# Kernel optimization log

Measured on AMD Instinct MI355X. Metric: run time of the kernel, lower is better.

Reference implementation:

```python
import jax, jax.numpy as jnp
import numpy as np

PC_MIN = jnp.array([0.0, -39.68, -3.0], jnp.float32)
VOX = jnp.array([0.16, 0.16, 4.0], jnp.float32)
NX, NY = 432, 496  # grid cells in x and y (z grid size is 1)
MAXP = 32          # max points per pillar


def setup_inputs():
    key = jax.random.key(0)
    ks = jax.random.split(key, 16)
    B, N = 2, 16000
    u = jax.random.uniform(ks[0], (B, N, 4), dtype=jnp.float32)
    # points uniformly spread over the point-cloud range, intensity in [0,1)
    points = jnp.stack([u[..., 0] * 69.12, u[..., 1] * 79.36 - 39.68,
                        u[..., 2] * 4.0 - 3.0, u[..., 3]], axis=-1)

    def cw(k, co, ci):
        return jax.random.normal(k, (co, ci, 3, 3), jnp.float32) / np.float32(np.sqrt(ci * 9.0))

    def cws(k, L, c):
        return jax.random.normal(k, (L, c, c, 3, 3), jnp.float32) / np.float32(np.sqrt(c * 9.0))

    def st(k, shape):
        k1, k2 = jax.random.split(k)
        return (1.0 + 0.1 * jax.random.normal(k1, shape, jnp.float32),
                0.1 * jax.random.normal(k2, shape, jnp.float32))

    vfe_w = 0.1 * jax.random.normal(ks[1], (64, 10), jnp.float32)
    vfe_s, vfe_t = st(ks[2], (64,))
    b1_w0 = cw(ks[3], 4, 64);   b1_s0, b1_t0 = st(ks[4], (4,))
    b1_w = cws(ks[5], 3, 4);    b1_s, b1_t = st(ks[6], (3, 4))
    b2_w0 = cw(ks[7], 16, 4);   b2_s0, b2_t0 = st(ks[8], (16,))
    b2_w = cws(ks[9], 5, 16);   b2_s, b2_t = st(ks[10], (5, 16))
    b3_w0 = cw(ks[11], 64, 16); b3_s0, b3_t0 = st(ks[12], (64,))
    b3_w = cws(ks[13], 5, 64);  b3_s, b3_t = st(ks[14], (5, 64))
    return dict(points=points, vfe_w=vfe_w, vfe_s=vfe_s, vfe_t=vfe_t,
                b1_w0=b1_w0, b1_s0=b1_s0, b1_t0=b1_t0, b1_w=b1_w, b1_s=b1_s, b1_t=b1_t,
                b2_w0=b2_w0, b2_s0=b2_s0, b2_t0=b2_t0, b2_w=b2_w, b2_s=b2_s, b2_t=b2_t,
                b3_w0=b3_w0, b3_s0=b3_s0, b3_t0=b3_t0, b3_w=b3_w, b3_s=b3_s, b3_t=b3_t)


def _voxelize_vfe_scatter(points, vfe_w, vfe_s, vfe_t):
    """Hard voxelization (hash-bucket by pillar coord, pad to MAXP) + PillarVFE + scatter to BEV canvas."""
    B, N, C = points.shape
    V = B * N  # worst case: every point its own pillar
    pts = points.reshape(V, C)
    cid = jnp.floor((pts[:, :3] - PC_MIN) / VOX).astype(jnp.int32)
    cid = jnp.clip(cid, 0, jnp.array([NX - 1, NY - 1, 0], jnp.int32))
    bidx = jnp.repeat(jnp.arange(B, dtype=jnp.int32), N)
    # linear pillar id: b*NY*NX + y*NX + x  (z grid dim is 1 -> z idx always 0)
    gid = bidx * (NY * NX) + cid[:, 1] * NX + cid[:, 0]
    order = jnp.argsort(gid)  # stable -> preserves per-pillar point order
    g = gid[order]; p = pts[order]; c = cid[order]
    pos = jnp.arange(V, dtype=jnp.int32)
    flag = jnp.concatenate([jnp.ones((1,), bool), g[1:] != g[:-1]])
    vidx = jnp.cumsum(flag) - 1                                 # dense pillar index
    rank = pos - jax.lax.cummax(jnp.where(flag, pos, 0), axis=0)  # slot within pillar
    keep = rank < MAXP
    voxels = jnp.zeros((V, MAXP, C), points.dtype).at[vidx, rank].set(p, mode='drop')
    num = jnp.zeros((V,), jnp.int32).at[vidx].add(keep.astype(jnp.int32))
    OOB = B * NY * NX
    pillar_gid = jnp.full((V,), OOB, jnp.int32).at[vidx].set(g)  # unused slots stay out-of-bounds
    pillar_c = jnp.zeros((V, 3), jnp.int32).at[vidx].set(c)
    # PillarVFE features: [x,y,z,r, cluster offset(3), center offset(3)] = 10
    denom = jnp.maximum(num, 1).astype(points.dtype)[:, None]
    mean = jnp.zeros((V, 3), points.dtype).at[vidx].add(p[:, :3] * keep[:, None]) / denom
    f_cluster = voxels[:, :, :3] - mean[:, None, :]
    center = pillar_c.astype(points.dtype) * VOX + (VOX * 0.5 + PC_MIN)
    f_center = voxels[:, :, :3] - center[:, None, :]
    mask = (jnp.arange(MAXP)[None, :] < num[:, None])[:, :, None].astype(points.dtype)
    feat = jnp.concatenate([voxels, f_cluster, f_center], axis=-1) * mask  # (V, 32, 10)
    x = jnp.einsum('vpc,oc->vpo', feat, vfe_w)        # PFN linear (no bias)
    x = jax.nn.relu(x * vfe_s + vfe_t)                # eval-mode BN folded to scale/shift
    pillar = x.max(axis=1)                            # (V, 64) max over points
    canvas = jnp.zeros((B * NY * NX, 64), points.dtype).at[pillar_gid].set(pillar, mode='drop')
    return canvas.reshape(B, NY, NX, 64).transpose(0, 3, 1, 2)  # (B, 64, NY, NX)


def _conv_bn_relu(x, w, s, t):
    y = jax.lax.conv_general_dilated(x, w, (1, 1), [(1, 1), (1, 1)],
                                     dimension_numbers=('NCHW', 'OIHW', 'NCHW'))
    return jax.nn.relu(y * s[None, :, None, None] + t[None, :, None, None])


def _block(x, w0, s0, t0, ws, ss, ts):
    x = _conv_bn_relu(x, w0, s0, t0)
    for i in range(ws.shape[0]):  # fixed small layer count
        x = _conv_bn_relu(x, ws[i], ss[i], ts[i])
    return x


def reference(points, vfe_w, vfe_s, vfe_t,
              b1_w0, b1_s0, b1_t0, b1_w, b1_s, b1_t,
              b2_w0, b2_s0, b2_t0, b2_w, b2_s, b2_t,
              b3_w0, b3_s0, b3_t0, b3_w, b3_s, b3_t):
    bev = _voxelize_vfe_scatter(points, vfe_w, vfe_s, vfe_t)
    x1 = _block(bev, b1_w0, b1_s0, b1_t0, b1_w, b1_s, b1_t)
    x2 = _block(x1, b2_w0, b2_s0, b2_t0, b2_w, b2_s, b2_t)
    x3 = _block(x2, b3_w0, b3_s0, b3_t0, b3_w, b3_s, b3_t)
    # no deblocks (cfg lacks UPSAMPLE_STRIDES) -> concat raw block outputs: 4+16+64 = 84 ch
    return jnp.concatenate([x1, x2, x3], axis=1)  # (B, 84, 496, 432)
```

## Files before the change

kernel.cpp:

```cpp
#include <hip/hip_runtime.h>
#include <math.h>

static constexpr int H = 496, W = 432, Bn = 2, Np = 16000;
static constexpr int HW = H * W;

typedef __bf16 bf16x8 __attribute__((ext_vector_type(8)));
typedef float f32x16 __attribute__((ext_vector_type(16)));

__device__ inline void bin_xy(float px, float py, int& ix, int& iy) {
  ix = (int)floorf(px * 6.25f);
  iy = (int)floorf((py + 39.68f) * 6.25f);
  ix = min(max(ix, 0), W - 1);
  iy = min(max(iy, 0), H - 1);
}

__global__ __launch_bounds__(256)
void count_kernel(const float* __restrict__ pts, int* __restrict__ cnt,
                  float* __restrict__ sums) {
  int p = blockIdx.x * blockDim.x + threadIdx.x;
  if (p >= Bn * Np) return;
  float px = pts[p * 4 + 0], py = pts[p * 4 + 1], pz = pts[p * 4 + 2];
  int b = p / Np;
  int ix, iy;
  bin_xy(px, py, ix, iy);
  int gid = b * HW + iy * W + ix;
  atomicAdd(&cnt[gid], 1);
  atomicAdd(&sums[3 * gid + 0], px);
  atomicAdd(&sums[3 * gid + 1], py);
  atomicAdd(&sums[3 * gid + 2], pz);
}

__global__ __launch_bounds__(256)
void vfe_kernel(const float* __restrict__ pts, const int* __restrict__ cnt,
                const float* __restrict__ sums, const float* __restrict__ vw,
                const float* __restrict__ vs, const float* __restrict__ vt,
                float* __restrict__ out) {
  int tid = blockIdx.x * blockDim.x + threadIdx.x;
  if (tid >= Bn * Np * 64) return;
  int o = tid & 63;
  int p = tid >> 6;
  int b = p / Np;
  float px = pts[p * 4 + 0], py = pts[p * 4 + 1];
  float pz = pts[p * 4 + 2], pr = pts[p * 4 + 3];
  int ix, iy;
  bin_xy(px, py, ix, iy);
  int gid = b * HW + iy * W + ix;
  int n = cnt[gid];
  float denom = (float)max(n, 1);
  float mx = sums[3 * gid + 0] / denom;
  float my = sums[3 * gid + 1] / denom;
  float mz = sums[3 * gid + 2] / denom;
  float cx = (float)ix * 0.16f + 0.08f;
  float cy = (float)iy * 0.16f + (0.08f - 39.68f);
  float f[10] = {px, py, pz, pr, px - mx, py - my, pz - mz,
                 px - cx, py - cy, pz + 1.0f};
  const float* wr = vw + o * 10;
  float d = 0.f;
#pragma unroll
  for (int c = 0; c < 10; c++) d += f[c] * wr[c];
  float val = d * vs[o] + vt[o];
  val = fmaxf(val, 0.f);
  if (n < 32) val = fmaxf(val, fmaxf(vt[o], 0.f));
  unsigned int* dst = (unsigned int*)(out + (size_t)b * (84 * HW) +
                                      (size_t)(20 + o) * HW + (size_t)iy * W + ix);
  atomicMax(dst, __float_as_uint(val));
}

template <int CI, int COT>
__global__ __launch_bounds__(256)
void conv3x3(const float* __restrict__ in, int in_bs, const float* __restrict__ w,
             const float* __restrict__ s, const float* __restrict__ t,
             float* __restrict__ out, int out_bs, int npix) {
  int pix = blockIdx.x * blockDim.x + threadIdx.x;
  if (pix >= npix) return;
  int b = pix / HW;
  int rem = pix - b * HW;
  int y = rem / W;
  int x = rem - y * W;
  int co0 = blockIdx.y * COT;
  const float* inb = in + (size_t)b * in_bs;

  int offs[9];
  bool okm[9];
#pragma unroll
  for (int ky = 0; ky < 3; ky++) {
    int yy = y + ky - 1;
    bool yok = (unsigned)yy < (unsigned)H;
#pragma unroll
    for (int kx = 0; kx < 3; kx++) {
      int xx = x + kx - 1;
      okm[ky * 3 + kx] = yok && ((unsigned)xx < (unsigned)W);
      offs[ky * 3 + kx] = yy * W + xx;
    }
  }
  float acc[COT];
#pragma unroll
  for (int i = 0; i < COT; i++) acc[i] = 0.f;
  for (int ci = 0; ci < CI; ci++) {
    const float* ip = inb + (size_t)ci * HW;
    float iv[9];
#pragma unroll
    for (int k = 0; k < 9; k++) iv[k] = okm[k] ? ip[offs[k]] : 0.f;
    const float* wp = w + ((size_t)co0 * CI + ci) * 9;
#pragma unroll
    for (int cg = 0; cg < COT; cg++) {
      const float* wc = wp + (size_t)cg * CI * 9;
#pragma unroll
      for (int k = 0; k < 9; k++) acc[cg] = fmaf(iv[k], wc[k], acc[cg]);
    }
  }
  float* ob = out + (size_t)b * out_bs + (size_t)rem;
#pragma unroll
  for (int cg = 0; cg < COT; cg++) {
    float v = acc[cg] * s[co0 + cg] + t[co0 + cg];
    ob[(size_t)(co0 + cg) * HW] = fmaxf(v, 0.f);
  }
}

__global__ __launch_bounds__(256)
void prepack(const float* __restrict__ w0, const float* __restrict__ ws,
             __bf16* __restrict__ wt) {
  int idx = blockIdx.x * 256 + threadIdx.x;
  const int E0 = 64 * 144, EN = 64 * 576;
  if (idx < E0) {
    int blk = idx >> 9, rem = idx & 511;
    int tp = blk >> 1, nt = blk & 1;
    int co = nt * 32 + (rem >> 4);
    int ci = rem & 15;
    int ky = tp / 3, kx = tp - ky * 3;
    wt[idx] = (__bf16)w0[((co * 16 + ci) * 3 + ky) * 3 + kx];
  } else {
    int j = idx - E0;
    if (j >= 5 * EN) return;
    int n = j / EN, rr = j - n * EN;
    int blk = rr >> 9, rem = rr & 511;
    int tpkc = blk >> 1, nt = blk & 1;
    int tp = tpkc >> 2, kc = tpkc & 3;
    int co = nt * 32 + (rem >> 4);
    int ci = kc * 16 + (rem & 15);
    int ky = tp / 3, kx = tp - ky * 3;
    wt[idx] = (__bf16)ws[n * 36864 + ((co * 64 + ci) * 3 + ky) * 3 + kx];
  }
}

__global__ __launch_bounds__(256)
void cvt_nhwc16(const float* __restrict__ x2, __bf16* __restrict__ n16) {
  int q = blockIdx.x * 256 + threadIdx.x;
  if (q >= Bn * HW) return;
  int b = q / HW;
  int p = q - b * HW;
  const float* x2b = x2 + (size_t)b * 84 * HW;
  __bf16* nb = n16 + (size_t)b * 84 * HW * 2;
  __bf16 v[16];
#pragma unroll
  for (int ci = 0; ci < 16; ci++) v[ci] = (__bf16)x2b[(size_t)ci * HW + p];
  *(bf16x8*)(nb + (size_t)p * 16) = *(bf16x8*)v;
  *(bf16x8*)(nb + (size_t)p * 16 + 8) = *(bf16x8*)(v + 8);
}

template <int CI, bool FINAL>
__global__ __launch_bounds__(256, 3)
void mconv(const __bf16* __restrict__ in, size_t in_bstride,
           const __bf16* __restrict__ wt, const float* __restrict__ s,
           const float* __restrict__ t, __bf16* __restrict__ outb,
           size_t outb_bstride, float* __restrict__ outf, size_t outf_bstride) {
  constexpr int KC = CI / 16;
  constexpr int PADW = (CI == 64) ? 72 : 24;
  constexpr int HALO_B = 324 * PADW * 2;
  constexpr int TRAN_B = FINAL ? 128 * 66 * 4 : 0;
  constexpr int SMEM_B = HALO_B > TRAN_B ? HALO_B : TRAN_B;
  __shared__ __align__(16) char smem[SMEM_B];
  __bf16* hl = (__bf16*)smem;

  const int tid = threadIdx.x;
  const int bz = blockIdx.y;
  const int ty = blockIdx.x / 27, tx = blockIdx.x - ty * 27;
  const int y0 = ty * 16, x0 = tx * 16;
  in += (size_t)bz * in_bstride;

  constexpr int NCH = CI / 8;
  constexpr int TOT = 324 * NCH;
  for (int q = tid; q < TOT; q += 256) {
    int hp = q / NCH, c8 = q - hp * NCH;
    int hy = hp / 18, hx = hp - hy * 18;
    int gy = y0 - 1 + hy, gx = x0 - 1 + hx;
    int4 v = {0, 0, 0, 0};
    if ((unsigned)gy < (unsigned)H && (unsigned)gx < (unsigned)W)
      v = *(const int4*)(in + (size_t)(gy * W + gx) * CI + c8 * 8);
    *(int4*)(hl + hp * PADW + c8 * 8) = v;
  }
  __syncthreads();

  const int lane = tid & 63;
  const int wv = tid >> 6;
  const int col = lane & 31, half = lane >> 5;
  const int ly0 = 4 * wv + (col >> 4);
  const int lx = col & 15;

  f32x16 z = {0.f, 0.f, 0.f, 0.f, 0.f, 0.f, 0.f, 0.f,
              0.f, 0.f, 0.f, 0.f, 0.f, 0.f, 0.f, 0.f};
  f32x16 a00 = z, a01 = z, a10 = z, a11 = z;

  const int laneoff = col * 16 + half * 8;
  const __bf16* wbase = wt + laneoff;

#pragma unroll
  for (int tp = 0; tp < 9; ++tp) {
    const __bf16* a0r = hl + ((ly0 + tp / 3) * 18 + lx + tp % 3) * PADW + half * 8;
    const __bf16* a1r = a0r + 2 * 18 * PADW;
    const __bf16* bb = wbase + ((tp * KC) << 10);
#pragma unroll
    for (int kc = 0; kc < KC; ++kc) {
      bf16x8 af0 = *(const bf16x8*)(a0r + kc * 16);
      bf16x8 af1 = *(const bf16x8*)(a1r + kc * 16);
      bf16x8 b0 = *(const bf16x8*)(bb + (kc << 10));
      bf16x8 b1 = *(const bf16x8*)(bb + (kc << 10) + 512);
      a00 = __builtin_amdgcn_mfma_f32_32x32x16_bf16(af0, b0, a00, 0, 0, 0);
      a01 = __builtin_amdgcn_mfma_f32_32x32x16_bf16(af0, b1, a01, 0, 0, 0);
      a10 = __builtin_amdgcn_mfma_f32_32x32x16_bf16(af1, b0, a10, 0, 0, 0);
      a11 = __builtin_amdgcn_mfma_f32_32x32x16_bf16(af1, b1, a11, 0, 0, 0);
    }
  }

  float s0 = s[col], t0v = t[col], s1 = s[col + 32], t1v = t[col + 32];
  if constexpr (!FINAL) {
    __bf16* ob = outb + (size_t)bz * outb_bstride;
#pragma unroll
    for (int r = 0; r < 16; ++r) {
      int row = (r & 3) + 8 * (r >> 2) + 4 * half;
      int py = y0 + 4 * wv + (row >> 4);
      int px = x0 + (row & 15);
      size_t gp0 = (size_t)py * W + px;
      size_t gp1 = gp0 + (size_t)2 * W;
      ob[gp0 * 64 + col] = (__bf16)fmaxf(a00[r] * s0 + t0v, 0.f);
      ob[gp0 * 64 + col + 32] = (__bf16)fmaxf(a01[r] * s1 + t1v, 0.f);
      ob[gp1 * 64 + col] = (__bf16)fmaxf(a10[r] * s0 + t0v, 0.f);
      ob[gp1 * 64 + col + 32] = (__bf16)fmaxf(a11[r] * s1 + t1v, 0.f);
    }
  } else {
    float* of = outf + (size_t)bz * outf_bstride;
    float* tl = (float*)smem;
    for (int h = 0; h < 2; ++h) {
      __syncthreads();
      if ((wv >> 1) == h) {
        int wl = wv & 1;
#pragma unroll
        for (int r = 0; r < 16; ++r) {
          int row = (r & 3) + 8 * (r >> 2) + 4 * half;
          int lp0 = (4 * wl + (row >> 4)) * 16 + (row & 15);
          int lp1 = lp0 + 32;
          tl[lp0 * 66 + col] = fmaxf(a00[r] * s0 + t0v, 0.f);
          tl[lp0 * 66 + col + 32] = fmaxf(a01[r] * s1 + t1v, 0.f);
          tl[lp1 * 66 + col] = fmaxf(a10[r] * s0 + t0v, 0.f);
          tl[lp1 * 66 + col + 32] = fmaxf(a11[r] * s1 + t1v, 0.f);
        }
      }
      __syncthreads();
      for (int e = tid; e < 128 * 64; e += 256) {
        int co = e >> 7, mtl = e & 127;
        of[(size_t)co * HW + (size_t)(y0 + h * 8 + (mtl >> 4)) * W +
           (x0 + (mtl & 15))] = tl[mtl * 66 + co];
      }
    }
  }
}

extern "C" void kernel_launch(void* const* d_in, const int* in_sizes, int n_in,
                              void* d_out, int out_size, void* d_ws, size_t ws_size,
                              hipStream_t stream) {
  const float* pts  = (const float*)d_in[0];
  const float* vw   = (const float*)d_in[1];
  const float* vs   = (const float*)d_in[2];
  const float* vt   = (const float*)d_in[3];
  const float* b1w0 = (const float*)d_in[4];
  const float* b1s0 = (const float*)d_in[5];
  const float* b1t0 = (const float*)d_in[6];
  const float* b1w  = (const float*)d_in[7];
  const float* b1s  = (const float*)d_in[8];
  const float* b1t  = (const float*)d_in[9];
  const float* b2w0 = (const float*)d_in[10];
  const float* b2s0 = (const float*)d_in[11];
  const float* b2t0 = (const float*)d_in[12];
  const float* b2w  = (const float*)d_in[13];
  const float* b2s  = (const float*)d_in[14];
  const float* b2t  = (const float*)d_in[15];
  const float* b3w0 = (const float*)d_in[16];
  const float* b3s0 = (const float*)d_in[17];
  const float* b3t0 = (const float*)d_in[18];
  const float* b3w  = (const float*)d_in[19];
  const float* b3s  = (const float*)d_in[20];
  const float* b3t  = (const float*)d_in[21];
  float* out = (float*)d_out;

  float* wsf = (float*)d_ws;
  int* cnt = (int*)wsf;
  float* sums = wsf + (size_t)2 * HW;
  float* s16a = wsf;
  float* s16b = wsf + (size_t)32 * HW;
  __bf16* ppA = (__bf16*)d_ws;
  __bf16* Wt = (__bf16*)((char*)d_ws + (size_t)64 * HW * 4);

  prepack<<<756, 256, 0, stream>>>(b3w0, b3w, Wt);

  hipMemsetAsync(out + (size_t)20 * HW, 0, (size_t)64 * HW * sizeof(float), stream);
  hipMemsetAsync(out + (size_t)(84 + 20) * HW, 0, (size_t)64 * HW * sizeof(float),
                 stream);
  hipMemsetAsync(cnt, 0, (size_t)8 * HW * sizeof(float), stream);

  count_kernel<<<(Bn * Np + 255) / 256, 256, 0, stream>>>(pts, cnt, sums);
  vfe_kernel<<<(Bn * Np * 64 + 255) / 256, 256, 0, stream>>>(pts, cnt, sums, vw, vs,
                                                             vt, out);

  const int g2 = (2 * HW + 255) / 256;
  dim3 blk(256);
  float* canvas = out + (size_t)20 * HW;

  conv3x3<64, 4><<<dim3(g2, 1), blk, 0, stream>>>(canvas, 84 * HW, b1w0, b1s0, b1t0,
                                                  s16a, 4 * HW, 2 * HW);
  conv3x3<4, 4><<<dim3(g2, 1), blk, 0, stream>>>(s16a, 4 * HW, b1w + 0 * 144,
                                                 b1s + 0, b1t + 0, s16b, 4 * HW,
                                                 2 * HW);
  conv3x3<4, 4><<<dim3(g2, 1), blk, 0, stream>>>(s16b, 4 * HW, b1w + 1 * 144,
                                                 b1s + 4, b1t + 4, s16a, 4 * HW,
                                                 2 * HW);
  conv3x3<4, 4><<<dim3(g2, 1), blk, 0, stream>>>(s16a, 4 * HW, b1w + 2 * 144,
                                                 b1s + 8, b1t + 8, out, 84 * HW,
                                                 2 * HW);

  conv3x3<4, 16><<<dim3(g2, 1), blk, 0, stream>>>(out, 84 * HW, b2w0, b2s0, b2t0,
                                                  s16a, 16 * HW, 2 * HW);
  conv3x3<16, 16><<<dim3(g2, 1), blk, 0, stream>>>(s16a, 16 * HW, b2w + 0 * 2304,
                                                   b2s + 0, b2t + 0, s16b, 16 * HW,
                                                   2 * HW);
  conv3x3<16, 16><<<dim3(g2, 1), blk, 0, stream>>>(s16b, 16 * HW, b2w + 1 * 2304,
                                                   b2s + 16, b2t + 16, s16a, 16 * HW,
                                                   2 * HW);
  conv3x3<16, 16><<<dim3(g2, 1), blk, 0, stream>>>(s16a, 16 * HW, b2w + 2 * 2304,
                                                   b2s + 32, b2t + 32, s16b, 16 * HW,
                                                   2 * HW);
  conv3x3<16, 16><<<dim3(g2, 1), blk, 0, stream>>>(s16b, 16 * HW, b2w + 3 * 2304,
                                                   b2s + 48, b2t + 48, s16a, 16 * HW,
                                                   2 * HW);
  conv3x3<16, 16><<<dim3(g2, 1), blk, 0, stream>>>(s16a, 16 * HW, b2w + 4 * 2304,
                                                   b2s + 64, b2t + 64, out + 4 * HW,
                                                   84 * HW, 2 * HW);

  __bf16* n16 = (__bf16*)canvas;
  const size_t canv_s = (size_t)84 * HW * 2;
  const size_t ppa_s = (size_t)64 * HW;
  cvt_nhwc16<<<(Bn * HW + 255) / 256, 256, 0, stream>>>(out + (size_t)4 * HW, n16);
  dim3 mg(31 * 27, Bn);
  mconv<16, false><<<mg, blk, 0, stream>>>(n16, canv_s, Wt, b3s0, b3t0, ppA, ppa_s,
                                           nullptr, 0);
  mconv<64, false><<<mg, blk, 0, stream>>>(ppA, ppa_s, Wt + 9216 + 0 * 36864,
                                           b3s + 0, b3t + 0, n16, canv_s, nullptr,
                                           0);
  mconv<64, false><<<mg, blk, 0, stream>>>(n16, canv_s, Wt + 9216 + 1 * 36864,
                                           b3s + 64, b3t + 64, ppA, ppa_s, nullptr,
                                           0);
  mconv<64, false><<<mg, blk, 0, stream>>>(ppA, ppa_s, Wt + 9216 + 2 * 36864,
                                           b3s + 128, b3t + 128, n16, canv_s,
                                           nullptr, 0);
  mconv<64, false><<<mg, blk, 0, stream>>>(n16, canv_s, Wt + 9216 + 3 * 36864,
                                           b3s + 192, b3t + 192, ppA, ppa_s,
                                           nullptr, 0);
  mconv<64, true><<<mg, blk, 0, stream>>>(ppA, ppa_s, Wt + 9216 + 4 * 36864,
                                          b3s + 256, b3t + 256, nullptr, 0, canvas,
                                          (size_t)84 * HW);
}
```

Before: 866.1 us.

## Scatter VFE to NHWC canvas and fuse last block-2 conv with bf16 NHWC conversion

The VFE now scatters into a pixel-major (NHWC) fp32 canvas in workspace, so each point's 64 atomicMax updates land in contiguous memory instead of 64 planes HW apart. A new conv64_nhwc kernel reads that canvas with float4 loads for the first block-1 conv. The last block-2 conv now also writes the bf16 NHWC copy directly, which removes the separate cvt_nhwc16 pass. The cost is a larger workspace and a memset of a 128*HW canvas, and the conv64 weight reads stay strided and scalar.

Result: slower. 909.6 us (+5.0%).

```diff
diff --git a/kernel.cpp b/kernel.cpp
--- a/kernel.cpp
+++ b/kernel.cpp
@@ -34,7 +34,7 @@
 void vfe_kernel(const float* __restrict__ pts, const int* __restrict__ cnt,
                 const float* __restrict__ sums, const float* __restrict__ vw,
                 const float* __restrict__ vs, const float* __restrict__ vt,
-                float* __restrict__ out) {
+                float* __restrict__ canv) {
   int tid = blockIdx.x * blockDim.x + threadIdx.x;
   if (tid >= Bn * Np * 64) return;
   int o = tid & 63;
@@ -61,9 +61,60 @@
   float val = d * vs[o] + vt[o];
   val = fmaxf(val, 0.f);
   if (n < 32) val = fmaxf(val, fmaxf(vt[o], 0.f));
-  unsigned int* dst = (unsigned int*)(out + (size_t)b * (84 * HW) +
-                                      (size_t)(20 + o) * HW + (size_t)iy * W + ix);
+  unsigned int* dst = (unsigned int*)(canv + (size_t)gid * 64 + o);
   atomicMax(dst, __float_as_uint(val));
+}
+
+__global__ __launch_bounds__(256)
+void conv64_nhwc(const float* __restrict__ canv, const float* __restrict__ w0,
+                 const float* __restrict__ s, const float* __restrict__ t,
+                 float* __restrict__ out4) {
+  int pix = blockIdx.x * 256 + threadIdx.x;
+  if (pix >= Bn * HW) return;
+  int b = pix / HW;
+  int rem = pix - b * HW;
+  int y = rem / W;
+  int x = rem - y * W;
+  const float* cb = canv + (size_t)b * HW * 64;
+  float a0 = 0.f, a1 = 0.f, a2 = 0.f, a3 = 0.f;
+#pragma unroll
+  for (int ky = 0; ky < 3; ky++) {
+    int yy = y + ky - 1;
+    if ((unsigned)yy >= (unsigned)H) continue;
+#pragma unroll
+    for (int kx = 0; kx < 3; kx++) {
+      int xx = x + kx - 1;
+      if ((unsigned)xx >= (unsigned)W) continue;
+      const float* cp = cb + (size_t)(yy * W + xx) * 64;
+      const float* wp = w0 + (ky * 3 + kx);
+#pragma unroll
+      for (int c4 = 0; c4 < 16; c4++) {
+        float4 v = *(const float4*)(cp + c4 * 4);
+        int ci = c4 * 4;
+        a0 = fmaf(v.x, wp[0 * 576 + (ci + 0) * 9], a0);
+        a1 = fmaf(v.x, wp[1 * 576 + (ci + 0) * 9], a1);
+        a2 = fmaf(v.x, wp[2 * 576 + (ci + 0) * 9], a2);
+        a3 = fmaf(v.x, wp[3 * 576 + (ci + 0) * 9], a3);
+        a0 = fmaf(v.y, wp[0 * 576 + (ci + 1) * 9], a0);
+        a1 = fmaf(v.y, wp[1 * 576 + (ci + 1) * 9], a1);
+        a2 = fmaf(v.y, wp[2 * 576 + (ci + 1) * 9], a2);
+        a3 = fmaf(v.y, wp[3 * 576 + (ci + 1) * 9], a3);
+        a0 = fmaf(v.z, wp[0 * 576 + (ci + 2) * 9], a0);
+        a1 = fmaf(v.z, wp[1 * 576 + (ci + 2) * 9], a1);
+        a2 = fmaf(v.z, wp[2 * 576 + (ci + 2) * 9], a2);
+        a3 = fmaf(v.z, wp[3 * 576 + (ci + 2) * 9], a3);
+        a0 = fmaf(v.w, wp[0 * 576 + (ci + 3) * 9], a0);
+        a1 = fmaf(v.w, wp[1 * 576 + (ci + 3) * 9], a1);
+        a2 = fmaf(v.w, wp[2 * 576 + (ci + 3) * 9], a2);
+        a3 = fmaf(v.w, wp[3 * 576 + (ci + 3) * 9], a3);
+      }
+    }
+  }
+  float* ob = out4 + (size_t)b * 4 * HW + rem;
+  ob[0 * HW] = fmaxf(a0 * s[0] + t[0], 0.f);
+  ob[1 * HW] = fmaxf(a1 * s[1] + t[1], 0.f);
+  ob[2 * HW] = fmaxf(a2 * s[2] + t[2], 0.f);
+  ob[3 * HW] = fmaxf(a3 * s[3] + t[3], 0.f);
 }
 
 template <int CI, int COT>
@@ -103,18 +154,72 @@
     for (int k = 0; k < 9; k++) iv[k] = okm[k] ? ip[offs[k]] : 0.f;
     const float* wp = w + ((size_t)co0 * CI + ci) * 9;
 #pragma unroll
-    for (int cg = 0; cg < COT; cg++) {
-      const float* wc = wp + (size_t)cg * CI * 9;
-#pragma unroll
-      for (int k = 0; k < 9; k++) acc[cg] = fmaf(iv[k], wc[k], acc[cg]);
+    for (int cg_ = 0; cg_ < COT; cg_++) {
+      const float* wc = wp + (size_t)cg_ * CI * 9;
+#pragma unroll
+      for (int k = 0; k < 9; k++) acc[cg_] = fmaf(iv[k], wc[k], acc[cg_]);
     }
   }
   float* ob = out + (size_t)b * out_bs + (size_t)rem;
 #pragma unroll
-  for (int cg = 0; cg < COT; cg++) {
-    float v = acc[cg] * s[co0 + cg] + t[co0 + cg];
-    ob[(size_t)(co0 + cg) * HW] = fmaxf(v, 0.f);
-  }
+  for (int cg_ = 0; cg_ < COT; cg_++) {
+    float v = acc[cg_] * s[co0 + cg_] + t[co0 + cg_];
+    ob[(size_t)(co0 + cg_) * HW] = fmaxf(v, 0.f);
+  }
+}
+
+__global__ __launch_bounds__(256)
+void conv16_dual(const float* __restrict__ in, const float* __restrict__ w,
+                 const float* __restrict__ s, const float* __restrict__ t,
+                 float* __restrict__ out, __bf16* __restrict__ n16) {
+  int pix = blockIdx.x * blockDim.x + threadIdx.x;
+  if (pix >= Bn * HW) return;
+  int b = pix / HW;
+  int rem = pix - b * HW;
+  int y = rem / W;
+  int x = rem - y * W;
+  const float* inb = in + (size_t)b * 16 * HW;
+
+  int offs[9];
+  bool okm[9];
+#pragma unroll
+  for (int ky = 0; ky < 3; ky++) {
+    int yy = y + ky - 1;
+    bool yok = (unsigned)yy < (unsigned)H;
+#pragma unroll
+    for (int kx = 0; kx < 3; kx++) {
+      int xx = x + kx - 1;
+      okm[ky * 3 + kx] = yok && ((unsigned)xx < (unsigned)W);
+      offs[ky * 3 + kx] = yy * W + xx;
+    }
+  }
+  float acc[16];
+#pragma unroll
+  for (int i = 0; i < 16; i++) acc[i] = 0.f;
+  for (int ci = 0; ci < 16; ci++) {
+    const float* ip = inb + (size_t)ci * HW;
+    float iv[9];
+#pragma unroll
+    for (int k = 0; k < 9; k++) iv[k] = okm[k] ? ip[offs[k]] : 0.f;
+    const float* wp = w + (size_t)ci * 9;
+#pragma unroll
+    for (int cg_ = 0; cg_ < 16; cg_++) {
+      const float* wc = wp + (size_t)cg_ * 16 * 9;
+#pragma unroll
+      for (int k = 0; k < 9; k++) acc[cg_] = fmaf(iv[k], wc[k], acc[cg_]);
+    }
+  }
+  float* ob = out + (size_t)b * 84 * HW + (size_t)rem;
+  __bf16 vv[16];
+#pragma unroll
+  for (int cg_ = 0; cg_ < 16; cg_++) {
+    float v = fmaxf(acc[cg_] * s[cg_] + t[cg_], 0.f);
+    ob[(size_t)cg_ * HW] = v;
+    vv[cg_] = (__bf16)v;
+  }
+  __bf16* nb = n16 + (size_t)b * (84 * HW * 2) + (size_t)rem * 16;
+  *(bf16x8*)nb = *(bf16x8*)vv;
+  *(bf16x8*)(nb + 8) = *(bf16x8*)(vv + 8);
 }
 
 __global__ __launch_bounds__(256)
@@ -141,21 +246,6 @@
     int ky = tp / 3, kx = tp - ky * 3;
     wt[idx] = (__bf16)ws[n * 36864 + ((co * 64 + ci) * 3 + ky) * 3 + kx];
   }
-}
-
-__global__ __launch_bounds__(256)
-void cvt_nhwc16(const float* __restrict__ x2, __bf16* __restrict__ n16) {
-  int q = blockIdx.x * 256 + threadIdx.x;
-  if (q >= Bn * HW) return;
-  int b = q / HW;
-  int p = q - b * HW;
-  const float* x2b = x2 + (size_t)b * 84 * HW;
-  __bf16* nb = n16 + (size_t)b * 84 * HW * 2;
-  __bf16 v[16];
-#pragma unroll
-  for (int ci = 0; ci < 16; ci++) v[ci] = (__bf16)x2b[(size_t)ci * HW + p];
-  *(bf16x8*)(nb + (size_t)p * 16) = *(bf16x8*)v;
-  *(bf16x8*)(nb + (size_t)p * 16 + 8) = *(bf16x8*)(v + 8);
 }
 
 template <int CI, bool FINAL>
@@ -297,26 +387,23 @@
   float* sums = wsf + (size_t)2 * HW;
   float* s16a = wsf;
   float* s16b = wsf + (size_t)32 * HW;
+  float* canv = wsf + (size_t)64 * HW;
   __bf16* ppA = (__bf16*)d_ws;
-  __bf16* Wt = (__bf16*)((char*)d_ws + (size_t)64 * HW * 4);
+  __bf16* Wt = (__bf16*)((char*)d_ws + (size_t)192 * HW * 4);
 
   prepack<<<756, 256, 0, stream>>>(b3w0, b3w, Wt);
 
-  hipMemsetAsync(out + (size_t)20 * HW, 0, (size_t)64 * HW * sizeof(float), stream);
-  hipMemsetAsync(out + (size_t)(84 + 20) * HW, 0, (size_t)64 * HW * sizeof(float),
-                 stream);
   hipMemsetAsync(cnt, 0, (size_t)8 * HW * sizeof(float), stream);
+  hipMemsetAsync(canv, 0, (size_t)128 * HW * sizeof(float), stream);
 
   count_kernel<<<(Bn * Np + 255) / 256, 256, 0, stream>>>(pts, cnt, sums);
   vfe_kernel<<<(Bn * Np * 64 + 255) / 256, 256, 0, stream>>>(pts, cnt, sums, vw, vs,
-                                                             vt, out);
+                                                             vt, canv);
 
   const int g2 = (2 * HW + 255) / 256;
   dim3 blk(256);
-  float* canvas = out + (size_t)20 * HW;
-
-  conv3x3<64, 4><<<dim3(g2, 1), blk, 0, stream>>>(canvas, 84 * HW, b1w0, b1s0, b1t0,
-                                                  s16a, 4 * HW, 2 * HW);
+
+  conv64_nhwc<<<g2, blk, 0, stream>>>(canv, b1w0, b1s0, b1t0, s16a);
   conv3x3<4, 4><<<dim3(g2, 1), blk, 0, stream>>>(s16a, 4 * HW, b1w + 0 * 144,
                                                  b1s + 0, b1t + 0, s16b, 4 * HW,
                                                  2 * HW);
@@ -327,6 +414,7 @@
                                                  b1s + 8, b1t + 8, out, 84 * HW,
                                                  2 * HW);
 
+  __bf16* n16 = (__bf16*)(out + (size_t)20 * HW);
   conv3x3<4, 16><<<dim3(g2, 1), blk, 0, stream>>>(out, 84 * HW, b2w0, b2s0, b2t0,
                                                   s16a, 16 * HW, 2 * HW);
   conv3x3<16, 16><<<dim3(g2, 1), blk, 0, stream>>>(s16a, 16 * HW, b2w + 0 * 2304,
@@ -341,14 +429,11 @@
   conv3x3<16, 16><<<dim3(g2, 1), blk, 0, stream>>>(s16b, 16 * HW, b2w + 3 * 2304,
                                                    b2s + 48, b2t + 48, s16a, 16 * HW,
                                                    2 * HW);
-  conv3x3<16, 16><<<dim3(g2, 1), blk, 0, stream>>>(s16a, 16 * HW, b2w + 4 * 2304,
-                                                   b2s + 64, b2t + 64, out + 4 * HW,
-                                                   84 * HW, 2 * HW);
-
-  __bf16* n16 = (__bf16*)canvas;
+  conv16_dual<<<g2, blk, 0, stream>>>(s16a, b2w + 4 * 2304, b2s + 64, b2t + 64,
+                                      out + 4 * HW, n16);
+
   const size_t canv_s = (size_t)84 * HW * 2;
   const size_t ppa_s = (size_t)64 * HW;
-  cvt_nhwc16<<<(Bn * HW + 255) / 256, 256, 0, stream>>>(out + (size_t)4 * HW, n16);
   dim3 mg(31 * 27, Bn);
   mconv<16, false><<<mg, blk, 0, stream>>>(n16, canv_s, Wt, b3s0, b3t0, ppA, ppa_s,
                                            nullptr, 0);
@@ -365,6 +450,6 @@
                                            b3s + 192, b3t + 192, ppA, ppa_s,
                                            nullptr, 0);
   mconv<64, true><<<mg, blk, 0, stream>>>(ppA, ppa_s, Wt + 9216 + 4 * 36864,
-                                          b3s + 256, b3t + 256, nullptr, 0, canvas,
-                                          (size_t)84 * HW);
-}
+                                          b3s + 256, b3t + 256, nullptr, 0,
+                                          out + (size_t)20 * HW, (size_t)84 * HW);
+}
```
